# Kernel optimization log

Measured on AMD Instinct MI355X. Metric: run time of the kernel, lower is better.

The kernel has to match this reference:

```python
import jax, jax.numpy as jnp
import numpy as np
from jax import lax

N, CIN, COUT, T, V = 32, 64, 128, 256, 25
IC = COUT // 4
EPS = 1e-5


def setup_inputs() -> dict:
    key = jax.random.key(0)
    ks = jax.random.split(key, 16)
    rn = lambda k, shape, s=0.05: jax.random.normal(k, shape, jnp.float32) * s
    inp = {
        'x': jax.random.normal(ks[0], (N, CIN, T, V), jnp.float32),
        'A': rn(ks[1], (V, V), 0.2),
        'w1': rn(ks[2], (IC, CIN)), 'b1': rn(ks[3], (IC,), 0.01),
        'w2': rn(ks[4], (IC, CIN)), 'b2': rn(ks[5], (IC,), 0.01),
        'w3': rn(ks[6], (COUT, CIN)), 'b3': rn(ks[7], (COUT,), 0.01),
        'w4': rn(ks[8], (COUT, CIN)), 'b4': rn(ks[9], (COUT,), 0.01),
        'bn1_g': jnp.ones((COUT,)), 'bn1_b': jnp.zeros((COUT,)),
        'bn1_m': rn(ks[10], (COUT,), 0.1), 'bn1_v': jnp.ones((COUT,)),
        'wt': rn(ks[11], (COUT, COUT, 9, 1)), 'bt': rn(ks[12], (COUT,), 0.01),
        'bn2_g': jnp.ones((COUT,)), 'bn2_b': jnp.zeros((COUT,)),
        'bn2_m': rn(ks[13], (COUT,), 0.1), 'bn2_v': jnp.ones((COUT,)),
        'wr': rn(ks[14], (COUT, CIN)), 'br': rn(ks[15], (COUT,), 0.01),
        'bnr_g': jnp.ones((COUT,)), 'bnr_b': jnp.zeros((COUT,)),
        'bnr_m': jnp.zeros((COUT,)), 'bnr_v': jnp.ones((COUT,)),
    }
    return inp


def _conv1x1(x, w, b):
    # 1x1 Conv2d over (T,V): pure channel mix. x: [N,C,T,V], w: [O,C]
    return jnp.einsum('oc,nctv->notv', w, x) + b[None, :, None, None]


def _bn(x, g, b, m, v):
    # BatchNorm2d in eval mode (running stats)
    scale = g / jnp.sqrt(v + EPS)
    return x * scale[None, :, None, None] + (b - m * scale)[None, :, None, None]


def _forward(x, A, w1, b1, w2, b2, w3, b3, w4, b4,
             bn1_g, bn1_b, bn1_m, bn1_v, wt, bt,
             bn2_g, bn2_b, bn2_m, bn2_v, wr, br,
             bnr_g, bnr_b, bnr_m, bnr_v):
    n, _, t, v = x.shape
    cout = w3.shape[0]
    ic = cout // 4
    x1 = _conv1x1(x, w1, b1).mean(axis=2)  # [N,IC,V]
    x2 = _conv1x1(x, w2, b2).mean(axis=2)  # [N,IC,V]
    a = jax.nn.softmax(x1[..., :, None] - x2[..., None, :], axis=-1)  # [N,IC,V,V]
    x3 = _conv1x1(x, w3, b3).reshape(n, 4, ic, t, v)
    y = jnp.einsum('ncuv,nmctv->nmctu', a, x3).reshape(n, cout, t, v)
    y = y + jnp.einsum('uv,nctv->nctu', A, _conv1x1(x, w4, b4))
    # tcn: BN -> ReLU -> Conv2d (9,1) pad (4,0) -> BN
    y = jax.nn.relu(_bn(y, bn1_g, bn1_b, bn1_m, bn1_v))
    y = lax.conv_general_dilated(
        y, wt, window_strides=(1, 1), padding=[(4, 4), (0, 0)],
        dimension_numbers=('NCHW', 'OIHW', 'NCHW')) + bt[None, :, None, None]
    y = _bn(y, bn2_g, bn2_b, bn2_m, bn2_v)
    # residual branch (in_channels != out_channels): 1x1 conv + BN
    res = _bn(_conv1x1(x, wr, br), bnr_g, bnr_b, bnr_m, bnr_v)
    return jax.nn.relu(y + res)


def reference(x, A, w1, b1, w2, b2, w3, b3, w4, b4,
              bn1_g, bn1_b, bn1_m, bn1_v, wt, bt,
              bn2_g, bn2_b, bn2_m, bn2_v, wr, br,
              bnr_g, bnr_b, bnr_m, bnr_v):
    return _forward(x, A, w1, b1, w2, b2, w3, b3, w4, b4,
                    bn1_g, bn1_b, bn1_m, bn1_v, wt, bt,
                    bn2_g, bn2_b, bn2_m, bn2_v, wr, br,
                    bnr_g, bnr_b, bnr_m, bnr_v)
```

## Files before the change

### kernel.cpp

```cpp
#include <hip/hip_runtime.h>
#include <hip/hip_bf16.h>

typedef unsigned short u16;
typedef unsigned int u32;
typedef unsigned long long u64;
typedef __attribute__((ext_vector_type(8))) short short8;
typedef __attribute__((ext_vector_type(4))) float f32x4;

#define DI __device__ __forceinline__

DI float b2f(u16 v){ u32 u = ((u32)v) << 16; float f; __builtin_memcpy(&f, &u, 4); return f; }
DI u16 f2bu(float f){ __hip_bfloat16 h = __float2bfloat16(f); u16 u; __builtin_memcpy(&u, &h, 2); return u; }

DI void gll16(const u16* g, u16* l){
  __builtin_amdgcn_global_load_lds((const __attribute__((address_space(1))) void*)g,
                                   (__attribute__((address_space(3))) void*)l, 16, 0, 0);
}

__global__ __launch_bounds__(256) void kprep(const float* __restrict__ x, u16* __restrict__ xT){
  __shared__ u16 tile[128*72];
  const int xb = blockIdx.x, n = blockIdx.y, tid = threadIdx.x;
  const int x0 = xb*128;
  const int ci = tid>>2, part = tid&3;
  const float* src = x + ((size_t)(n*64+ci))*6400 + x0 + part*32;
  #pragma unroll
  for (int i=0;i<8;i++){
    float4 f = ((const float4*)src)[i];
    const int col = part*32 + i*4;
    tile[(col+0)*72+ci] = f2bu(f.x);
    tile[(col+1)*72+ci] = f2bu(f.y);
    tile[(col+2)*72+ci] = f2bu(f.z);
    tile[(col+3)*72+ci] = f2bu(f.w);
  }
  __syncthreads();
  const int row = tid>>1, half = tid&1;
  short8* dst = (short8*)(xT + ((size_t)n*6400 + x0 + row)*64 + half*32);
  const short8* s8 = (const short8*)(tile + row*72 + half*32);
  #pragma unroll
  for (int i=0;i<4;i++) dst[i] = s8[i];
}

__global__ __launch_bounds__(256) void kzero(float* __restrict__ xm){
  const int i = blockIdx.x*1024 + threadIdx.x*4;
  float4 z = {0.f,0.f,0.f,0.f};
  *(float4*)(xm + i) = z;
}

__global__ __launch_bounds__(256) void kmean(const u16* __restrict__ xT, float* __restrict__ xm){
  __shared__ float part[4][1600];
  const int seg = blockIdx.x, n = blockIdx.y, tid = threadIdx.x;
  const int tg = tid>>6, c = tid&63;
  float acc[25];
  #pragma unroll
  for (int v=0;v<25;v++) acc[v]=0.f;
  for (int t = seg*32 + tg; t < seg*32 + 32; t += 4){
    const u16* base = xT + ((size_t)n*6400 + t*25)*64 + c;
    #pragma unroll
    for (int v=0;v<25;v++) acc[v] += b2f(base[v*64]);
  }
  #pragma unroll
  for (int v=0;v<25;v++) part[tg][v*64+c] = acc[v];
  __syncthreads();
  for (int idx = tid; idx < 1600; idx += 256){
    const int v = idx>>6, cc = idx&63;
    const float m = part[0][idx]+part[1][idx]+part[2][idx]+part[3][idx];
    atomicAdd(&xm[(n*64+cc)*25+v], m*(1.f/256.f));
  }
}

__global__ __launch_bounds__(64) void kp(const float* __restrict__ xm, const float* __restrict__ w2,
                                         const float* __restrict__ b2p, const float* __restrict__ Ab,
                                         float* __restrict__ p, float* __restrict__ rsA){
  const int c = blockIdx.x, n = blockIdx.y, lane = threadIdx.x;
  __shared__ float sc[32];
  __shared__ float red[2];
  float neg = 0.f;
  if (lane < 25){
    float acc = b2p[c];
    for (int k = 0; k < 64; k++) acc += w2[c*64 + k] * xm[(n*64 + k)*25 + lane];
    neg = -acc;
    sc[lane] = neg;
  }
  __syncthreads();
  if (lane == 0){
    float m = sc[0];
    for (int i = 1; i < 25; i++) m = fmaxf(m, sc[i]);
    red[0] = m;
  }
  __syncthreads();
  float e = 0.f;
  if (lane < 25){ e = expf(neg - red[0]); sc[lane] = e; }
  __syncthreads();
  if (lane == 0){
    float ssum = 0.f;
    for (int i = 0; i < 25; i++) ssum += sc[i];
    red[1] = ssum;
  }
  __syncthreads();
  if (lane < 25) p[(n*32 + c)*25 + lane] = e / red[1];
  if (n == 0 && c == 0 && lane < 25){
    float r = 0.f;
    for (int v = 0; v < 25; v++) r += Ab[lane*25 + v];
    rsA[lane] = r;
  }
}

__global__ __launch_bounds__(256) void kxa(const u16* __restrict__ xT, const float* __restrict__ Ab,
                                           u16* __restrict__ xA){
  __shared__ float xl[200*68];
  __shared__ float al[625];
  const int tc = blockIdx.x, n = blockIdx.y, tid = threadIdx.x;
  const int x0t = tc * 200;
  for (int i = tid; i < 625; i += 256) al[i] = Ab[i];
  for (int idx = tid; idx < 1600; idx += 256){
    const int r = idx>>3, i = idx&7;
    short8 v = *(const short8*)(xT + ((size_t)n*6400 + x0t + r)*64 + i*8);
    float* dst = xl + r*68 + i*8;
    #pragma unroll
    for (int e=0;e<8;e++) dst[e] = b2f((u16)v[e]);
  }
  __syncthreads();
  if (tid < 200){
    const int t_ = tid / 25, u = tid % 25;
    float acc[64];
    #pragma unroll
    for (int k = 0; k < 64; k++) acc[k] = 0.f;
    const float* arow = al + u*25;
    for (int v = 0; v < 25; v++){
      const float a = arow[v];
      const float* xr = xl + (t_*25 + v)*68;
      #pragma unroll
      for (int k = 0; k < 64; k++) acc[k] += a * xr[k];
    }
    u16* dst = xA + ((size_t)n*6400 + x0t + tid)*64;
    #pragma unroll
    for (int k = 0; k < 64; k += 4){
      u64 pk = (u64)f2bu(acc[k]) | ((u64)f2bu(acc[k+1])<<16)
             | ((u64)f2bu(acc[k+2])<<32) | ((u64)f2bu(acc[k+3])<<48);
      *(u64*)(dst + k) = pk;
    }
  }
}

__global__ __launch_bounds__(256) void kwt(const float* __restrict__ wt, u16* __restrict__ wtb){
  const int o = blockIdx.x*256 + threadIdx.x;
  const int dt = o >> 14, rem = o & 16383;
  wtb[o] = f2bu(wt[rem*9 + dt]);
}

__global__ __launch_bounds__(256) void kwr(const float* __restrict__ wrw, const float* __restrict__ g2,
                                           const float* __restrict__ v2, const float* __restrict__ gr,
                                           const float* __restrict__ vr, u16* __restrict__ wrb){
  const int o = blockIdx.x*256 + threadIdx.x;
  const int co = o >> 6;
  const float E0 = g2[co]*rsqrtf(v2[co]+1e-5f);
  const float R0 = gr[co]*rsqrtf(vr[co]+1e-5f);
  wrb[o] = f2bu(wrw[o]*R0/E0);
}

__global__ __launch_bounds__(256) void khpad(u16* __restrict__ h){
  const int n = blockIdx.x, side = blockIdx.y, tid = threadIdx.x;
  short8* base = (short8*)(h + ((size_t)n*6600 + (side ? 6500 : 0))*128);
  short8 z = {0,0,0,0,0,0,0,0};
  for (int i = tid; i < 1600; i += 256) base[i] = z;
}

__global__ __launch_bounds__(256) void ks(const u16* __restrict__ xT, const float* __restrict__ w3,
                                          const float* __restrict__ p, float* __restrict__ s){
  __shared__ __align__(16) char smem[53248];
  __shared__ float pL[800];
  u16* aL = (u16*)smem;
  u16* bL = (u16*)(smem + 18432);
  float* z3 = (float*)smem;
  const int xb = blockIdx.x, n = blockIdx.y, tid = threadIdx.x;
  const int x0 = xb*100, t0 = xb*4;
  const int row = tid >> 1, half = tid & 1;
  {
    const float* src = w3 + row*64 + half*32;
    u16* dst = aL + row*72 + half*32;
    #pragma unroll
    for (int i=0;i<8;i++){
      float4 f = ((const float4*)src)[i];
      dst[i*4+0]=f2bu(f.x); dst[i*4+1]=f2bu(f.y); dst[i*4+2]=f2bu(f.z); dst[i*4+3]=f2bu(f.w);
    }
  }
  {
    short8* dst = (short8*)(bL + row*72 + half*32);
    if (row < 100){
      const short8* src = (const short8*)(xT + ((size_t)n*6400 + x0 + row)*64 + half*32);
      #pragma unroll
      for (int i=0;i<4;i++) dst[i] = src[i];
    } else {
      short8 z = {0,0,0,0,0,0,0,0};
      #pragma unroll
      for (int i=0;i<4;i++) dst[i] = z;
    }
  }
  for (int i = tid; i < 800; i += 256) pL[i] = p[n*800 + i];
  __syncthreads();
  const int wave = tid>>6, lane = tid&63, q = lane>>4, l = lane&15;
  const int wr = wave>>1, wc = wave&1;
  f32x4 acc[4][4];
  #pragma unroll
  for (int i=0;i<4;i++)
    #pragma unroll
    for (int j=0;j<4;j++){ f32x4 z0 = {0.f,0.f,0.f,0.f}; acc[i][j] = z0; }
  #pragma unroll
  for (int ksi = 0; ksi < 2; ksi++){
    const int kb = ksi*32 + q*8;
    short8 af[4], bf[4];
    #pragma unroll
    for (int i=0;i<4;i++) af[i] = *(const short8*)(aL + (wr*64 + i*16 + l)*72 + kb);
    #pragma unroll
    for (int j=0;j<4;j++) bf[j] = *(const short8*)(bL + (wc*64 + j*16 + l)*72 + kb);
    #pragma unroll
    for (int i=0;i<4;i++)
      #pragma unroll
      for (int j=0;j<4;j++)
        acc[i][j] = __builtin_amdgcn_mfma_f32_16x16x32_bf16(af[i], bf[j], acc[i][j], 0, 0, 0);
  }
  __syncthreads();
  #pragma unroll
  for (int i=0;i<4;i++){
    const int co0 = wr*64 + i*16 + q*4;
    #pragma unroll
    for (int j=0;j<4;j++){
      const int colx = wc*64 + j*16 + l;
      if (colx < 100){
        #pragma unroll
        for (int r=0;r<4;r++) z3[(co0 + r)*104 + colx] = acc[i][j][r];
      }
    }
  }
  __syncthreads();
  for (int idx = tid; idx < 512; idx += 256){
    const int co = idx >> 2, tt = idx & 3;
    const float* zr = z3 + co*104 + tt*25;
    const float* pr = pL + (co & 31)*25;
    float acc2 = 0.f;
    #pragma unroll
    for (int v=0; v<25; v++) acc2 += zr[v]*pr[v];
    s[((size_t)n*128 + co)*256 + t0 + tt] = acc2;
  }
}

__global__ __launch_bounds__(256) void ky(const u16* __restrict__ xA, const float* __restrict__ w4,
      const float* __restrict__ s, const float* __restrict__ b3, const float* __restrict__ b4,
      const float* __restrict__ g1, const float* __restrict__ bb1, const float* __restrict__ m1,
      const float* __restrict__ v1, const float* __restrict__ rsA, u16* __restrict__ h){
  __shared__ __align__(16) u16 aL[128*72];
  __shared__ __align__(16) u16 bL[128*72];
  __shared__ float A0[128], A1[128], A2[128];
  __shared__ float sF[1024];
  __shared__ float rs[32];
  const int xb = blockIdx.x, n = blockIdx.y, tid = threadIdx.x;
  const int x0 = xb*128, tlo = x0/25;
  const int row = tid >> 1, half = tid & 1;
  {
    const float* src = w4 + row*64 + half*32;
    u16* dst = aL + row*72 + half*32;
    #pragma unroll
    for (int i=0;i<8;i++){
      float4 f = ((const float4*)src)[i];
      dst[i*4+0]=f2bu(f.x); dst[i*4+1]=f2bu(f.y); dst[i*4+2]=f2bu(f.z); dst[i*4+3]=f2bu(f.w);
    }
  }
  {
    const short8* src = (const short8*)(xA + ((size_t)n*6400 + x0 + row)*64 + half*32);
    short8* dst = (short8*)(bL + row*72 + half*32);
    #pragma unroll
    for (int i=0;i<4;i++) dst[i] = src[i];
  }
  if (tid < 128){
    const float scv = g1[tid] * rsqrtf(v1[tid] + 1e-5f);
    A0[tid] = scv;
    A1[tid] = scv * b4[tid];
    A2[tid] = bb1[tid] - m1[tid] * scv;
  }
  if (tid < 32) rs[tid] = (tid < 25) ? rsA[tid] : 0.f;
  __syncthreads();
  for (int idx = tid; idx < 1024; idx += 256){
    const int co = idx >> 3, tt = idx & 7;
    const int t = tlo + tt;
    const float sv = (t < 256) ? s[((size_t)n*128 + co)*256 + t] : 0.f;
    sF[idx] = A0[co] * (sv + b3[co]) + A2[co];
  }
  const int wave = tid>>6, lane = tid&63, q = lane>>4, l = lane&15;
  const int wr = wave>>1, wc = wave&1;
  f32x4 acc[4][4];
  #pragma unroll
  for (int i=0;i<4;i++)
    #pragma unroll
    for (int j=0;j<4;j++){ f32x4 z0 = {0.f,0.f,0.f,0.f}; acc[i][j] = z0; }
  #pragma unroll
  for (int ksi = 0; ksi < 2; ksi++){
    const int kb = ksi*32 + q*8;
    short8 af[4], bf[4];
    #pragma unroll
    for (int i=0;i<4;i++) af[i] = *(const short8*)(aL + (wr*64 + i*16 + l)*72 + kb);
    #pragma unroll
    for (int j=0;j<4;j++) bf[j] = *(const short8*)(bL + (wc*64 + j*16 + l)*72 + kb);
    #pragma unroll
    for (int i=0;i<4;i++)
      #pragma unroll
      for (int j=0;j<4;j++)
        acc[i][j] = __builtin_amdgcn_mfma_f32_16x16x32_bf16(af[i], bf[j], acc[i][j], 0, 0, 0);
  }
  __syncthreads();
  #pragma unroll
  for (int i=0;i<4;i++){
    const int co0 = wr*64 + i*16 + q*4;
    #pragma unroll
    for (int j=0;j<4;j++){
      const int colx = wc*64 + j*16 + l;
      const int xg = x0 + colx;
      const int u = xg % 25, tt = xg/25 - tlo;
      const float rsu = rs[u];
      u64 pk = 0;
      #pragma unroll
      for (int r=0;r<4;r++){
        const int co = co0 + r;
        float y = A0[co]*acc[i][j][r] + A1[co]*rsu + sF[co*8 + tt];
        y = fmaxf(y, 0.f);
        pk |= ((u64)f2bu(y)) << (16*r);
      }
      *(u64*)(h + ((size_t)n*6600 + xg + 100)*128 + co0) = pk;
    }
  }
}

__global__ __launch_bounds__(1024, 4) void ktcn(const u16* __restrict__ h, const u16* __restrict__ wtb,
      const u16* __restrict__ wrb, const u16* __restrict__ xT,
      const float* __restrict__ bt, const float* __restrict__ g2, const float* __restrict__ bb2,
      const float* __restrict__ m2, const float* __restrict__ v2,
      const float* __restrict__ gr, const float* __restrict__ bbr, const float* __restrict__ mr,
      const float* __restrict__ vr, const float* __restrict__ brb,
      float* __restrict__ out){
  __shared__ __align__(16) char smem[149504];
  u16* hW = (u16*)smem;
  u16* Ab0 = (u16*)(smem + 83968);
  u16* Ab1 = (u16*)(smem + 116736);
  float* tr = (float*)smem;
  __shared__ float E0s[128], E1s[128];
  const int xb = blockIdx.x, n = blockIdx.y, tid = threadIdx.x;
  const int x0 = xb*128;
  const int wave = tid>>6, lane = tid&63, q = lane>>4, l = lane&15;
  const int wr2 = wave>>2, wc = wave&3;
  const u16* hbase = h + ((size_t)n*6600 + x0)*128;
  const u16* xtb = xT + ((size_t)n*6400 + x0)*64;

  #pragma unroll
  for (int it = 0; it < 5; ++it){
    const int ci = it*1024 + tid;
    const int r = ci >> 4, c = ci & 15;
    gll16(hbase + r*128 + ((c ^ (r & 15))<<3), hW + ((it*1024 + wave*64)<<3));
  }
  if (tid < 128){
    const int ci = 5120 + tid;
    const int r = ci >> 4, c = ci & 15;
    gll16(hbase + r*128 + ((c ^ (r & 15))<<3), hW + ((5120 + wave*64)<<3));
  }
  #pragma unroll
  for (int it = 0; it < 2; ++it){
    const int ci = it*1024 + tid;
    const int r = ci >> 4, c = ci & 15;
    gll16(wtb + r*128 + ((c ^ (r & 15))<<3), Ab0 + ((it*1024 + wave*64)<<3));
  }
  if (tid < 128){
    const float scv2 = g2[tid]*rsqrtf(v2[tid]+1e-5f);
    const float scvr = gr[tid]*rsqrtf(vr[tid]+1e-5f);
    E0s[tid] = scv2;
    E1s[tid] = scv2*bt[tid] + bb2[tid] - m2[tid]*scv2
             + (bbr[tid] - mr[tid]*scvr + scvr*brb[tid]);
  }
  f32x4 acc[2][2];
  #pragma unroll
  for (int i=0;i<2;i++)
    #pragma unroll
    for (int j=0;j<2;j++){ f32x4 z0 = {0.f,0.f,0.f,0.f}; acc[i][j] = z0; }
  __syncthreads();

  #pragma unroll 1
  for (int dt = 0; dt <= 9; ++dt){
    if (dt < 8){
      const u16* gA = wtb + (dt+1)*16384;
      u16* dA = (dt & 1) ? Ab0 : Ab1;
      #pragma unroll
      for (int it = 0; it < 2; ++it){
        const int ci = it*1024 + tid;
        const int r = ci >> 4, c = ci & 15;
        gll16(gA + r*128 + ((c ^ (r & 15))<<3), dA + ((it*1024 + wave*64)<<3));
      }
    } else if (dt == 8){
      {
        const int ci = tid;
        const int r = ci >> 3, c = ci & 7;
        gll16(wrb + r*64 + ((c ^ (r & 7))<<3), Ab1 + ((wave*64)<<3));
      }
      {
        const int ci = tid;
        const int r = ci >> 3, c = ci & 7;
        gll16(xtb + r*64 + ((c ^ (r & 7))<<3), Ab1 + 8192 + ((wave*64)<<3));
      }
    }
    if (dt < 9){
      const u16* A = (dt & 1) ? Ab1 : Ab0;
      #pragma unroll
      for (int ksi = 0; ksi < 4; ksi++){
        const int c0 = ksi*4 + q;
        short8 af[2], bf[2];
        #pragma unroll
        for (int i=0;i<2;i++){
          const int r = wr2*32 + i*16 + l;
          af[i] = *(const short8*)(A + (((r<<4) + (c0 ^ (r & 15)))<<3));
        }
        #pragma unroll
        for (int j=0;j<2;j++){
          const int r = dt*25 + wc*32 + j*16 + l;
          bf[j] = *(const short8*)(hW + (((r<<4) + (c0 ^ (r & 15)))<<3));
        }
        #pragma unroll
        for (int i=0;i<2;i++)
          #pragma unroll
          for (int j=0;j<2;j++)
            acc[i][j] = __builtin_amdgcn_mfma_f32_16x16x32_bf16(af[i], bf[j], acc[i][j], 0, 0, 0);
      }
    } else {
      const u16* A = Ab1;
      const u16* B = Ab1 + 8192;
      #pragma unroll
      for (int ksi = 0; ksi < 2; ksi++){
        const int c0 = ksi*4 + q;
        short8 af[2], bf[2];
        #pragma unroll
        for (int i=0;i<2;i++){
          const int r = wr2*32 + i*16 + l;
          af[i] = *(const short8*)(A + (((r<<3) + (c0 ^ (r & 7)))<<3));
        }
        #pragma unroll
        for (int j=0;j<2;j++){
          const int r = wc*32 + j*16 + l;
          bf[j] = *(const short8*)(B + (((r<<3) + (c0 ^ (r & 7)))<<3));
        }
        #pragma unroll
        for (int i=0;i<2;i++)
          #pragma unroll
          for (int j=0;j<2;j++)
            acc[i][j] = __builtin_amdgcn_mfma_f32_16x16x32_bf16(af[i], bf[j], acc[i][j], 0, 0, 0);
      }
    }
    __syncthreads();
  }

  #pragma unroll
  for (int i=0;i<2;i++){
    const int co0 = wr2*32 + i*16 + q*4;
    #pragma unroll
    for (int j=0;j<2;j++){
      const int colx = wc*32 + j*16 + l;
      #pragma unroll
      for (int r=0;r<4;r++){
        const float yv = E0s[co0+r]*acc[i][j][r] + E1s[co0+r];
        tr[(co0+r)*132 + colx] = fmaxf(yv, 0.f);
      }
    }
  }
  __syncthreads();
  {
    const int row = tid >> 3, seg = tid & 7;
    const float4* s4 = (const float4*)(tr + row*132 + seg*16);
    float4* d4 = (float4*)(out + ((size_t)n*128 + row)*6400 + x0 + seg*16);
    #pragma unroll
    for (int i = 0; i < 4; i++) d4[i] = s4[i];
  }
}

extern "C" void kernel_launch(void* const* d_in, const int* in_sizes, int n_in,
                              void* d_out, int out_size, void* d_ws, size_t ws_size,
                              hipStream_t stream){
  const float* x   = (const float*)d_in[0];
  const float* Ab  = (const float*)d_in[1];
  const float* w2  = (const float*)d_in[4];
  const float* b2p = (const float*)d_in[5];
  const float* w3  = (const float*)d_in[6];
  const float* b3  = (const float*)d_in[7];
  const float* w4  = (const float*)d_in[8];
  const float* b4  = (const float*)d_in[9];
  const float* g1  = (const float*)d_in[10];
  const float* bb1 = (const float*)d_in[11];
  const float* m1  = (const float*)d_in[12];
  const float* v1  = (const float*)d_in[13];
  const float* wt  = (const float*)d_in[14];
  const float* bt  = (const float*)d_in[15];
  const float* g2  = (const float*)d_in[16];
  const float* bb2 = (const float*)d_in[17];
  const float* m2  = (const float*)d_in[18];
  const float* v2  = (const float*)d_in[19];
  const float* wrw = (const float*)d_in[20];
  const float* brb = (const float*)d_in[21];
  const float* gr  = (const float*)d_in[22];
  const float* bbr = (const float*)d_in[23];
  const float* mr  = (const float*)d_in[24];
  const float* vr  = (const float*)d_in[25];
  float* out = (float*)d_out;

  char* ws = (char*)d_ws;
  float* xm  = (float*)(ws);
  float* p   = (float*)(ws + 204800);
  float* rsA = (float*)(ws + 307200);
  float* s   = (float*)(ws + 307712);
  u16* xT    = (u16*)(ws + 4502016);
  u16* xA    = (u16*)(ws + 30716416);
  u16* h     = (u16*)(ws + 56930816);
  u16* wtb   = (u16*)(ws + 110998016);
  u16* wrb   = (u16*)(ws + 111292928);

  kprep<<<dim3(50,32), 256, 0, stream>>>(x, xT);
  kzero<<<50, 256, 0, stream>>>(xm);
  kmean<<<dim3(8,32), 256, 0, stream>>>(xT, xm);
  kp<<<dim3(32,32), 64, 0, stream>>>(xm, w2, b2p, Ab, p, rsA);
  kxa<<<dim3(32,32), 256, 0, stream>>>(xT, Ab, xA);
  kwt<<<576, 256, 0, stream>>>(wt, wtb);
  kwr<<<32, 256, 0, stream>>>(wrw, g2, v2, gr, vr, wrb);
  khpad<<<dim3(32,2), 256, 0, stream>>>(h);
  ks<<<dim3(64,32), 256, 0, stream>>>(xT, w3, p, s);
  ky<<<dim3(50,32), 256, 0, stream>>>(xA, w4, s, b3, b4, g1, bb1, m1, v1, rsA, h);
  ktcn<<<dim3(50,32), 1024, 0, stream>>>(h, wtb, wrb, xT, bt, g2, bb2, m2, v2, gr, bbr, mr, vr, brb, out);
}
```

Before: 459.3 us.

## Read TCN weights directly from global memory and drop LDS staging and barriers

The temporal conv kernel no longer stages the weight taps and residual operands in double-buffered LDS. Each wave now loads its A fragments (and the residual's weight and input fragments) straight from global/L2 and runs the 9 taps without per-tap __syncthreads. The epilogue writes results straight to global instead of transposing through LDS. This shrinks shared memory and removes barriers, but it adds global-load latency inside the MFMA loop and leaves output stores less coalesced.

```diff
diff --git a/kernel.cpp b/kernel.cpp
--- a/kernel.cpp
+++ b/kernel.cpp
@@ -336,11 +336,7 @@
       const float* __restrict__ gr, const float* __restrict__ bbr, const float* __restrict__ mr,
       const float* __restrict__ vr, const float* __restrict__ brb,
       float* __restrict__ out){
-  __shared__ __align__(16) char smem[149504];
-  u16* hW = (u16*)smem;
-  u16* Ab0 = (u16*)(smem + 83968);
-  u16* Ab1 = (u16*)(smem + 116736);
-  float* tr = (float*)smem;
+  __shared__ __align__(16) u16 hW[328*128];
   __shared__ float E0s[128], E1s[128];
   const int xb = blockIdx.x, n = blockIdx.y, tid = threadIdx.x;
   const int x0 = xb*128;
@@ -360,12 +356,6 @@
     const int r = ci >> 4, c = ci & 15;
     gll16(hbase + r*128 + ((c ^ (r & 15))<<3), hW + ((5120 + wave*64)<<3));
   }
-  #pragma unroll
-  for (int it = 0; it < 2; ++it){
-    const int ci = it*1024 + tid;
-    const int r = ci >> 4, c = ci & 15;
-    gll16(wtb + r*128 + ((c ^ (r & 15))<<3), Ab0 + ((it*1024 + wave*64)<<3));
-  }
   if (tid < 128){
     const float scv2 = g2[tid]*rsqrtf(v2[tid]+1e-5f);
     const float scvr = gr[tid]*rsqrtf(vr[tid]+1e-5f);
@@ -380,76 +370,49 @@
     for (int j=0;j<2;j++){ f32x4 z0 = {0.f,0.f,0.f,0.f}; acc[i][j] = z0; }
   __syncthreads();
 
-  #pragma unroll 1
-  for (int dt = 0; dt <= 9; ++dt){
-    if (dt < 8){
-      const u16* gA = wtb + (dt+1)*16384;
-      u16* dA = (dt & 1) ? Ab0 : Ab1;
-      #pragma unroll
-      for (int it = 0; it < 2; ++it){
-        const int ci = it*1024 + tid;
-        const int r = ci >> 4, c = ci & 15;
-        gll16(gA + r*128 + ((c ^ (r & 15))<<3), dA + ((it*1024 + wave*64)<<3));
+  #pragma unroll 3
+  for (int dt = 0; dt < 9; ++dt){
+    const u16* gA = wtb + dt*16384;
+    #pragma unroll
+    for (int ksi = 0; ksi < 4; ksi++){
+      const int c0 = ksi*4 + q;
+      short8 af[2], bf[2];
+      #pragma unroll
+      for (int i=0;i<2;i++){
+        const int r = wr2*32 + i*16 + l;
+        af[i] = *(const short8*)(gA + r*128 + c0*8);
       }
-    } else if (dt == 8){
-      {
-        const int ci = tid;
-        const int r = ci >> 3, c = ci & 7;
-        gll16(wrb + r*64 + ((c ^ (r & 7))<<3), Ab1 + ((wave*64)<<3));
+      #pragma unroll
+      for (int j=0;j<2;j++){
+        const int r = dt*25 + wc*32 + j*16 + l;
+        bf[j] = *(const short8*)(hW + (((r<<4) + (c0 ^ (r & 15)))<<3));
       }
-      {
-        const int ci = tid;
-        const int r = ci >> 3, c = ci & 7;
-        gll16(xtb + r*64 + ((c ^ (r & 7))<<3), Ab1 + 8192 + ((wave*64)<<3));
-      }
-    }
-    if (dt < 9){
-      const u16* A = (dt & 1) ? Ab1 : Ab0;
-      #pragma unroll
-      for (int ksi = 0; ksi < 4; ksi++){
-        const int c0 = ksi*4 + q;
-        short8 af[2], bf[2];
+      #pragma unroll
+      for (int i=0;i<2;i++)
         #pragma unroll
-        for (int i=0;i<2;i++){
-          const int r = wr2*32 + i*16 + l;
-          af[i] = *(const short8*)(A + (((r<<4) + (c0 ^ (r & 15)))<<3));
-        }
-        #pragma unroll
-        for (int j=0;j<2;j++){
-          const int r = dt*25 + wc*32 + j*16 + l;
-          bf[j] = *(const short8*)(hW + (((r<<4) + (c0 ^ (r & 15)))<<3));
-        }
-        #pragma unroll
-        for (int i=0;i<2;i++)
-          #pragma unroll
-          for (int j=0;j<2;j++)
-            acc[i][j] = __builtin_amdgcn_mfma_f32_16x16x32_bf16(af[i], bf[j], acc[i][j], 0, 0, 0);
-      }
-    } else {
-      const u16* A = Ab1;
-      const u16* B = Ab1 + 8192;
-      #pragma unroll
-      for (int ksi = 0; ksi < 2; ksi++){
-        const int c0 = ksi*4 + q;
-        short8 af[2], bf[2];
-        #pragma unroll
-        for (int i=0;i<2;i++){
-          const int r = wr2*32 + i*16 + l;
-          af[i] = *(const short8*)(A + (((r<<3) + (c0 ^ (r & 7)))<<3));
-        }
-        #pragma unroll
-        for (int j=0;j<2;j++){
-          const int r = wc*32 + j*16 + l;
-          bf[j] = *(const short8*)(B + (((r<<3) + (c0 ^ (r & 7)))<<3));
-        }
-        #pragma unroll
-        for (int i=0;i<2;i++)
-          #pragma unroll
-          for (int j=0;j<2;j++)
-            acc[i][j] = __builtin_amdgcn_mfma_f32_16x16x32_bf16(af[i], bf[j], acc[i][j], 0, 0, 0);
-      }
-    }
-    __syncthreads();
+        for (int j=0;j<2;j++)
+          acc[i][j] = __builtin_amdgcn_mfma_f32_16x16x32_bf16(af[i], bf[j], acc[i][j], 0, 0, 0);
+    }
+  }
+  #pragma unroll
+  for (int ksi = 0; ksi < 2; ksi++){
+    const int c0 = ksi*4 + q;
+    short8 af[2], bf[2];
+    #pragma unroll
+    for (int i=0;i<2;i++){
+      const int r = wr2*32 + i*16 + l;
+      af[i] = *(const short8*)(wrb + r*64 + c0*8);
+    }
+    #pragma unroll
+    for (int j=0;j<2;j++){
+      const int r = wc*32 + j*16 + l;
+      bf[j] = *(const short8*)(xtb + r*64 + c0*8);
+    }
+    #pragma unroll
+    for (int i=0;i<2;i++)
+      #pragma unroll
+      for (int j=0;j<2;j++)
+        acc[i][j] = __builtin_amdgcn_mfma_f32_16x16x32_bf16(af[i], bf[j], acc[i][j], 0, 0, 0);
   }
 
   #pragma unroll
@@ -461,17 +424,9 @@
       #pragma unroll
       for (int r=0;r<4;r++){
         const float yv = E0s[co0+r]*acc[i][j][r] + E1s[co0+r];
-        tr[(co0+r)*132 + colx] = fmaxf(yv, 0.f);
+        out[((size_t)n*128 + co0 + r)*6400 + x0 + colx] = fmaxf(yv, 0.f);
       }
     }
-  }
-  __syncthreads();
-  {
-    const int row = tid >> 3, seg = tid & 7;
-    const float4* s4 = (const float4*)(tr + row*132 + seg*16);
-    float4* d4 = (float4*)(out + ((size_t)n*128 + row)*6400 + x0 + seg*16);
-    #pragma unroll
-    for (int i = 0; i < 4; i++) d4[i] = s4[i];
   }
 }
 
```

Result: slower. 596.8 us (+29.9%).
